# Kernel tuning notes

Measured on AMD Instinct MI355X. Metric: run time of the kernel, lower is better.

Reference implementation:

```python
import jax, jax.numpy as jnp
import numpy as np

NUM_HEADS = 16
KERNEL_SIZE = 13


def setup_inputs() -> dict:
    key = jax.random.key(0)
    ks = jax.random.split(key, 6)
    B, L, C = 4, 4096, 512
    H, K = NUM_HEADS, KERNEL_SIZE
    x = jax.random.normal(ks[0], (B, L, C), dtype=jnp.float32)
    qkv_w = jax.random.normal(ks[1], (C, 3 * C), dtype=jnp.float32) * 0.02
    qkv_b = jnp.zeros((3 * C,), dtype=jnp.float32)
    rpb = jax.random.normal(ks[2], (H, 2 * K - 1), dtype=jnp.float32) * 0.02
    proj_w = jax.random.normal(ks[3], (C, C), dtype=jnp.float32) * 0.02
    proj_b = jnp.zeros((C,), dtype=jnp.float32)
    return {"x": x, "qkv_w": qkv_w, "qkv_b": qkv_b, "rpb": rpb,
            "proj_w": proj_w, "proj_b": proj_b}


def reference(x, qkv_w, qkv_b, rpb, proj_w, proj_b):
    B, L, C = x.shape
    H, K = NUM_HEADS, KERNEL_SIZE
    hd = C // H
    scale = hd ** -0.5
    kh = K // 2

    # qkv projection -> q,k,v each [B,H,L,hd]
    qkv = (x @ qkv_w + qkv_b).reshape(B, L, 3, H, hd).transpose(2, 0, 3, 1, 4)
    q, k, v = qkv[0] * scale, qkv[1], qkv[2]

    # NATTEN window: start index clamped so window stays in-bounds
    pos = jnp.arange(L)
    ni = jnp.clip(pos - kh, 0, L - K)              # [L] window start per query
    idx = ni[:, None] + jnp.arange(K)[None, :]     # [L,K] key positions
    # rpb index: (key_pos - query_pos) + (K-1)
    rpb_idx = (ni - pos + (K - 1))[:, None] + jnp.arange(K)[None, :]  # [L,K]

    k_win = k[:, :, idx, :]                        # [B,H,L,K,hd]
    v_win = v[:, :, idx, :]                        # [B,H,L,K,hd]

    attn = jnp.einsum('bhld,bhlkd->bhlk', q, k_win) + rpb[:, rpb_idx][None]
    attn = jax.nn.softmax(attn, axis=-1)

    out = jnp.einsum('bhlk,bhlkd->bhld', attn, v_win)  # [B,H,L,hd]
    out = out.transpose(0, 2, 1, 3).reshape(B, L, C)
    return out @ proj_w + proj_b
```

## Files before the change

kernel.cpp:

```cpp
#include <hip/hip_runtime.h>
#include <hip/hip_bf16.h>
#include <stdint.h>


typedef __attribute__((ext_vector_type(8))) short short8;
typedef __attribute__((ext_vector_type(4))) float f32x4;
typedef __attribute__((ext_vector_type(8))) unsigned short u16x8;
typedef __attribute__((ext_vector_type(4))) float float4v;

#define NB 4
#define NL 4096
#define NC 512
#define NH 16
#define HD 32
#define KW 13
#define KHALF 6
#define NM (NB*NL)

__device__ __forceinline__ float b2f(unsigned short u) {
  union { unsigned int i; float f; } x; x.i = ((unsigned int)u) << 16; return x.f;
}
__device__ __forceinline__ unsigned short f2b(float f) {
  __hip_bfloat16 h = __float2bfloat16(f);
  return __builtin_bit_cast(unsigned short, h);
}
__device__ __forceinline__ void gll16(const unsigned short* g, unsigned short* l) {
  __builtin_amdgcn_global_load_lds(
      (const __attribute__((address_space(1))) void*)g,
      (__attribute__((address_space(3))) void*)l, 16, 0, 0);
}

__global__ __launch_bounds__(256) void cvt_f32_bf16(const float* __restrict__ in,
                                                    unsigned short* __restrict__ out) {
  long i = (long)blockIdx.x * 256 + threadIdx.x;
  const float4v* in4 = (const float4v*)in;
  float4v a = in4[i * 2];
  float4v b = in4[i * 2 + 1];
  u16x8 u;
  u[0] = f2b(a.x); u[1] = f2b(a.y); u[2] = f2b(a.z); u[3] = f2b(a.w);
  u[4] = f2b(b.x); u[5] = f2b(b.y); u[6] = f2b(b.z); u[7] = f2b(b.w);
  ((u16x8*)out)[i] = u;
}

__global__ __launch_bounds__(256) void transpose_bf16(const float* __restrict__ in,
                                                      unsigned short* __restrict__ out,
                                                      int R, int C) {
  __shared__ float t[32][33];
  int c0 = blockIdx.x * 32;
  int r0 = blockIdx.y * 32;
  int tx = threadIdx.x;
  int ty = threadIdx.y;
  #pragma unroll
  for (int i = ty; i < 32; i += 8)
    t[i][tx] = in[(long)(r0 + i) * C + c0 + tx];
  __syncthreads();
  #pragma unroll
  for (int i = ty; i < 32; i += 8)
    out[(long)(c0 + i) * R + r0 + tx] = f2b(t[tx][i]);
}


__device__ __forceinline__ void stage_half(const unsigned short* __restrict__ G,
                                           long rowBase, int K, int kt,
                                           unsigned short* ldsDst, int tid) {
  int r  = tid >> 3;
  int ch = (tid & 7) ^ (r & 7);
  const unsigned short* s0 = G + (rowBase + r) * (long)K + kt * 64 + ch * 8;
  gll16(s0, ldsDst + tid * 8);
  gll16(s0 + 64 * (long)K, ldsDst + 4096 + tid * 8);
}

#define BAR() __builtin_amdgcn_s_barrier()
#define LGK0() asm volatile("s_waitcnt lgkmcnt(0)" ::: "memory")
#define VM(N) asm volatile("s_waitcnt vmcnt(" #N ")" ::: "memory")

#define DS_A(ABASE, QM) do { \
  const char* _ba = (const char*)(ABASE); \
  _Pragma("unroll") for (int ii = 0; ii < 2; ++ii) { \
    int _row = wm*64 + ((QM)*2+ii)*16 + lr; \
    _Pragma("unroll") for (int kb = 0; kb < 2; ++kb) \
      af[ii][kb] = *(const short8*)(_ba + _row*128 + (((kb*4+lk) ^ lr7) * 16)); \
  } \
} while (0)

#define DS_B(BBASE, QN, BF) do { \
  const char* _bb = (const char*)(BBASE); \
  _Pragma("unroll") for (int jj = 0; jj < 2; ++jj) { \
    int _row = wn*64 + ((QN)*2+jj)*16 + lr; \
    _Pragma("unroll") for (int kb = 0; kb < 2; ++kb) \
      BF[jj][kb] = *(const short8*)(_bb + _row*128 + (((kb*4+lk) ^ lr7) * 16)); \
  } \
} while (0)

#define MMA(QM, QN, BF) do { \
  __builtin_amdgcn_s_setprio(1); \
  _Pragma("unroll") for (int ii = 0; ii < 2; ++ii) \
    _Pragma("unroll") for (int jj = 0; jj < 2; ++jj) \
      _Pragma("unroll") for (int kb = 0; kb < 2; ++kb) \
        acc[(QM)*2+ii][(QN)*2+jj] = __builtin_amdgcn_mfma_f32_16x16x32_bf16( \
            af[ii][kb], BF[jj][kb], acc[(QM)*2+ii][(QN)*2+jj], 0, 0, 0); \
  __builtin_amdgcn_s_setprio(0); \
} while (0)

template<int OUT_BF16>
__global__ __launch_bounds__(512, 2)
void gemm256(const unsigned short* __restrict__ A,
             const unsigned short* __restrict__ BT,
             const float* __restrict__ bias,
             void* __restrict__ Cout,
             int M, int N, int K, int tilesN) {
  __shared__ __align__(16) unsigned short lds[73728];

  int tid = threadIdx.x;
  int nwg = gridDim.x;
  int cpx = nwg >> 3;
  int wg  = ((int)blockIdx.x & 7) * cpx + ((int)blockIdx.x >> 3);
  int tm = wg / tilesN, tn = wg % tilesN;
  long mBase = (long)tm * 256;
  long nBase = (long)tn * 128;

  int lane = tid & 63, wave = tid >> 6;
  int wm = wave >> 1;
  int wn = wave & 1;
  int lr = lane & 15, lk = lane >> 4, lr7 = lr & 7;

  f32x4 acc[4][4];
  #pragma unroll
  for (int i = 0; i < 4; ++i)
    #pragma unroll
    for (int j = 0; j < 4; ++j) acc[i][j] = (f32x4){0.f, 0.f, 0.f, 0.f};

  short8 af[2][2], bf0[2][2], bf1[2][2];

  {
    unsigned short* A0 = lds;
    unsigned short* B0 = lds + 49152;
    unsigned short* A1 = lds + 16384;
    unsigned short* B1 = lds + 49152 + 8192;
    stage_half(A,  mBase,       K, 0, A0,        tid);
    stage_half(A,  mBase + 128, K, 0, A0 + 8192, tid);
    stage_half(BT, nBase,       K, 0, B0,        tid);
    stage_half(A,  mBase,       K, 1, A1,        tid);
    stage_half(A,  mBase + 128, K, 1, A1 + 8192, tid);
    stage_half(BT, nBase,       K, 1, B1,        tid);
  }
  VM(6);
  BAR();

  int bc = 0;
  #pragma unroll 1
  for (int kt = 0; kt < 8; ++kt) {
    int bs = bc == 0 ? 2 : bc - 1;
    unsigned short* A_cur = lds + bc * 16384;
    unsigned short* B_cur = lds + 49152 + bc * 8192;
    unsigned short* A_stg = lds + bs * 16384;
    unsigned short* B_stg = lds + 49152 + bs * 8192;
    bool st = (kt + 2) < 8;

    DS_A(A_cur, 0);
    DS_B(B_cur, 0, bf0);
    DS_B(B_cur, 1, bf1);
    if (st) {
      stage_half(A, mBase,       K, kt + 2, A_stg,        tid);
      stage_half(A, mBase + 128, K, kt + 2, A_stg + 8192, tid);
    }
    BAR(); LGK0();
    MMA(0, 0, bf0);
    MMA(0, 1, bf1);
    BAR();
    DS_A(A_cur, 1);
    if (st) stage_half(BT, nBase, K, kt + 2, B_stg, tid);
    BAR(); LGK0();
    MMA(1, 1, bf1);
    MMA(1, 0, bf0);
    if (st)              VM(6);
    else if (kt + 1 < 8) VM(0);
    BAR();
    bc = bc == 2 ? 0 : bc + 1;
  }

  long rowb = mBase + wm * 64 + (lane >> 4) * 4;
  int  colb = (int)nBase + wn * 64 + lr;
  if (OUT_BF16) {
    unsigned short* C = (unsigned short*)Cout;
    #pragma unroll
    for (int mi = 0; mi < 4; ++mi)
      #pragma unroll
      for (int nj = 0; nj < 4; ++nj) {
        int col = colb + nj * 16;
        float bv = bias[col];
        #pragma unroll
        for (int r = 0; r < 4; ++r)
          C[(rowb + mi * 16 + r) * (long)N + col] = f2b(acc[mi][nj][r] + bv);
      }
  } else {
    float* C = (float*)Cout;
    #pragma unroll
    for (int mi = 0; mi < 4; ++mi)
      #pragma unroll
      for (int nj = 0; nj < 4; ++nj) {
        int col = colb + nj * 16;
        float bv = bias[col];
        #pragma unroll
        for (int r = 0; r < 4; ++r)
          C[(rowb + mi * 16 + r) * (long)N + col] = acc[mi][nj][r] + bv;
      }
  }
}

__global__ __launch_bounds__(256)
void natt(const unsigned short* __restrict__ qkv, const float* __restrict__ rpb,
          unsigned short* __restrict__ out) {
  int tid = blockIdx.x * 256 + threadIdx.x;
  int h = tid & 15;
  int l = (tid >> 4) & (NL - 1);
  int b = tid >> 16;
  const float scale = 0.17677669529663687f;

  long qb = ((long)(b * NL + l) * 3) * NC + h * HD;
  float q[HD];
  {
    const u16x8* q8 = (const u16x8*)(qkv + qb);
    #pragma unroll
    for (int w = 0; w < 4; ++w) {
      u16x8 u = q8[w];
      #pragma unroll
      for (int e = 0; e < 8; ++e) q[w * 8 + e] = b2f(u[e]) * scale;
    }
  }

  int ni = l - KHALF;
  if (ni < 0) ni = 0;
  if (ni > NL - KW) ni = NL - KW;
  const float* rb = rpb + h * (2 * KW - 1) + (ni - l + KW - 1);

  float p[KW];
  float mx = -1e30f;
  #pragma unroll
  for (int j = 0; j < KW; ++j) {
    long kb = ((long)(b * NL + ni + j) * 3 + 1) * NC + h * HD;
    const u16x8* k8 = (const u16x8*)(qkv + kb);
    float s = 0.f;
    #pragma unroll
    for (int w = 0; w < 4; ++w) {
      u16x8 u = k8[w];
      #pragma unroll
      for (int e = 0; e < 8; ++e) s += q[w * 8 + e] * b2f(u[e]);
    }
    s += rb[j];
    p[j] = s;
    mx = fmaxf(mx, s);
  }

  float sum = 0.f;
  #pragma unroll
  for (int j = 0; j < KW; ++j) { p[j] = __expf(p[j] - mx); sum += p[j]; }
  float inv = 1.0f / sum;

  float o[HD];
  #pragma unroll
  for (int d = 0; d < HD; ++d) o[d] = 0.f;
  #pragma unroll
  for (int j = 0; j < KW; ++j) {
    long vb = ((long)(b * NL + ni + j) * 3 + 2) * NC + h * HD;
    const u16x8* v8 = (const u16x8*)(qkv + vb);
    float wj = p[j] * inv;
    #pragma unroll
    for (int w = 0; w < 4; ++w) {
      u16x8 u = v8[w];
      #pragma unroll
      for (int e = 0; e < 8; ++e) o[w * 8 + e] += wj * b2f(u[e]);
    }
  }

  unsigned short* op = out + (long)(b * NL + l) * NC + h * HD;
  #pragma unroll
  for (int w = 0; w < 4; ++w) {
    u16x8 u;
    #pragma unroll
    for (int e = 0; e < 8; ++e) u[e] = f2b(o[w * 8 + e]);
    *((u16x8*)(op + w * 8)) = u;
  }
}

extern "C" void kernel_launch(void* const* d_in, const int* in_sizes, int n_in,
                              void* d_out, int out_size, void* d_ws, size_t ws_size,
                              hipStream_t stream) {
  const float* x      = (const float*)d_in[0];
  const float* qkv_w  = (const float*)d_in[1];
  const float* qkv_b  = (const float*)d_in[2];
  const float* rpb    = (const float*)d_in[3];
  const float* proj_w = (const float*)d_in[4];
  const float* proj_b = (const float*)d_in[5];
  float* out = (float*)d_out;

  char* ws = (char*)d_ws;
  unsigned short* xb     = (unsigned short*)(ws);
  unsigned short* qkvwT  = (unsigned short*)(ws + 16777216);
  unsigned short* projwT = (unsigned short*)(ws + 18350080);
  unsigned short* qkvo   = (unsigned short*)(ws + 18874368);
  unsigned short* attno  = (unsigned short*)(ws + 69206016);

  cvt_f32_bf16<<<dim3(4096), dim3(256), 0, stream>>>(x, xb);
  transpose_bf16<<<dim3(48, 16), dim3(32, 8), 0, stream>>>(qkv_w, qkvwT, 512, 1536);
  transpose_bf16<<<dim3(16, 16), dim3(32, 8), 0, stream>>>(proj_w, projwT, 512, 512);
  gemm256<1><<<dim3(768), dim3(512), 0, stream>>>(xb, qkvwT, qkv_b, qkvo,
                                                  NM, 1536, 512, 12);
  natt<<<dim3(1024), dim3(256), 0, stream>>>(qkvo, rpb, attno);
  gemm256<0><<<dim3(256), dim3(512), 0, stream>>>(attno, projwT, proj_b, out,
                                                  NM, 512, 512, 4);
}
```

Measured before the change: 106.9 us.

## Replace 256x128 GEMM with 128x128 double-buffered tile and simpler k-loop

```diff
diff --git a/kernel.cpp b/kernel.cpp
--- a/kernel.cpp
+++ b/kernel.cpp
@@ -60,63 +60,78 @@
 }
 
 
-__device__ __forceinline__ void stage_half(const unsigned short* __restrict__ G,
+__device__ __forceinline__ void stage_tile(const unsigned short* __restrict__ G,
                                            long rowBase, int K, int kt,
                                            unsigned short* ldsDst, int tid) {
   int r  = tid >> 3;
   int ch = (tid & 7) ^ (r & 7);
   const unsigned short* s0 = G + (rowBase + r) * (long)K + kt * 64 + ch * 8;
-  gll16(s0, ldsDst + tid * 8);
-  gll16(s0 + 64 * (long)K, ldsDst + 4096 + tid * 8);
+  unsigned short* d0 = ldsDst + tid * 8;
+  #pragma unroll
+  for (int q = 0; q < 4; ++q)
+    gll16(s0 + (long)32 * q * K, d0 + 2048 * q);
 }
 
 #define BAR() __builtin_amdgcn_s_barrier()
-#define LGK0() asm volatile("s_waitcnt lgkmcnt(0)" ::: "memory")
+#define LGK0() do { asm volatile("s_waitcnt lgkmcnt(0)" ::: "memory"); \
+                    __builtin_amdgcn_sched_barrier(0); } while (0)
 #define VM(N) asm volatile("s_waitcnt vmcnt(" #N ")" ::: "memory")
 
-#define DS_A(ABASE, QM) do { \
+#define LDA(ABASE) do { \
   const char* _ba = (const char*)(ABASE); \
-  _Pragma("unroll") for (int ii = 0; ii < 2; ++ii) { \
-    int _row = wm*64 + ((QM)*2+ii)*16 + lr; \
+  _Pragma("unroll") for (int ii = 0; ii < 4; ++ii) { \
+    int _row = wm*64 + ii*16 + lr; \
     _Pragma("unroll") for (int kb = 0; kb < 2; ++kb) \
       af[ii][kb] = *(const short8*)(_ba + _row*128 + (((kb*4+lk) ^ lr7) * 16)); \
   } \
 } while (0)
 
-#define DS_B(BBASE, QN, BF) do { \
+#define LDB(BBASE) do { \
   const char* _bb = (const char*)(BBASE); \
-  _Pragma("unroll") for (int jj = 0; jj < 2; ++jj) { \
-    int _row = wn*64 + ((QN)*2+jj)*16 + lr; \
+  _Pragma("unroll") for (int jj = 0; jj < 4; ++jj) { \
+    int _row = wn*64 + jj*16 + lr; \
     _Pragma("unroll") for (int kb = 0; kb < 2; ++kb) \
-      BF[jj][kb] = *(const short8*)(_bb + _row*128 + (((kb*4+lk) ^ lr7) * 16)); \
+      bf[jj][kb] = *(const short8*)(_bb + _row*128 + (((kb*4+lk) ^ lr7) * 16)); \
   } \
 } while (0)
 
-#define MMA(QM, QN, BF) do { \
+#define MMA_ALL() do { \
   __builtin_amdgcn_s_setprio(1); \
-  _Pragma("unroll") for (int ii = 0; ii < 2; ++ii) \
-    _Pragma("unroll") for (int jj = 0; jj < 2; ++jj) \
+  _Pragma("unroll") for (int ii = 0; ii < 4; ++ii) \
+    _Pragma("unroll") for (int jj = 0; jj < 4; ++jj) \
       _Pragma("unroll") for (int kb = 0; kb < 2; ++kb) \
-        acc[(QM)*2+ii][(QN)*2+jj] = __builtin_amdgcn_mfma_f32_16x16x32_bf16( \
-            af[ii][kb], BF[jj][kb], acc[(QM)*2+ii][(QN)*2+jj], 0, 0, 0); \
+        acc[ii][jj] = __builtin_amdgcn_mfma_f32_16x16x32_bf16( \
+            af[ii][kb], bf[jj][kb], acc[ii][jj], 0, 0, 0); \
   __builtin_amdgcn_s_setprio(0); \
 } while (0)
 
+#define KTILE(AB, BB, KT, STG, VMARG) do { \
+  LDA(AB); LDB(BB); LGK0(); \
+  BAR(); \
+  if (STG) { \
+    stage_tile(Ag, mBase, K, (KT) + 2, AB, tid); \
+    stage_tile(Bg, nBase, K, (KT) + 2, BB, tid); \
+  } \
+  MMA_ALL(); \
+  VMARG; \
+  BAR(); \
+} while (0)
+
 template<int OUT_BF16>
-__global__ __launch_bounds__(512, 2)
-void gemm256(const unsigned short* __restrict__ A,
-             const unsigned short* __restrict__ BT,
+__global__ __launch_bounds__(256, 2)
+void gemm128(const unsigned short* __restrict__ Ag,
+             const unsigned short* __restrict__ Bg,
              const float* __restrict__ bias,
              void* __restrict__ Cout,
              int M, int N, int K, int tilesN) {
-  __shared__ __align__(16) unsigned short lds[73728];
+  __shared__ __align__(16) unsigned short lds[32768];
 
   int tid = threadIdx.x;
   int nwg = gridDim.x;
   int cpx = nwg >> 3;
   int wg  = ((int)blockIdx.x & 7) * cpx + ((int)blockIdx.x >> 3);
   int tm = wg / tilesN, tn = wg % tilesN;
-  long mBase = (long)tm * 256;
+  long mBase = (long)tm * 128;
   long nBase = (long)tn * 128;
 
   int lane = tid & 63, wave = tid >> 6;
@@ -124,59 +139,36 @@
   int wn = wave & 1;
   int lr = lane & 15, lk = lane >> 4, lr7 = lr & 7;
 
+  unsigned short* A0 = lds;
+  unsigned short* A1 = lds + 8192;
+  unsigned short* B0 = lds + 16384;
+  unsigned short* B1 = lds + 24576;
+
   f32x4 acc[4][4];
   #pragma unroll
   for (int i = 0; i < 4; ++i)
     #pragma unroll
     for (int j = 0; j < 4; ++j) acc[i][j] = (f32x4){0.f, 0.f, 0.f, 0.f};
 
-  short8 af[2][2], bf0[2][2], bf1[2][2];
-
-  {
-    unsigned short* A0 = lds;
-    unsigned short* B0 = lds + 49152;
-    unsigned short* A1 = lds + 16384;
-    unsigned short* B1 = lds + 49152 + 8192;
-    stage_half(A,  mBase,       K, 0, A0,        tid);
-    stage_half(A,  mBase + 128, K, 0, A0 + 8192, tid);
-    stage_half(BT, nBase,       K, 0, B0,        tid);
-    stage_half(A,  mBase,       K, 1, A1,        tid);
-    stage_half(A,  mBase + 128, K, 1, A1 + 8192, tid);
-    stage_half(BT, nBase,       K, 1, B1,        tid);
-  }
-  VM(6);
+  short8 af[4][2], bf[4][2];
+
+  stage_tile(Ag, mBase, K, 0, A0, tid);
+  stage_tile(Bg, nBase, K, 0, B0, tid);
+  stage_tile(Ag, mBase, K, 1, A1, tid);
+  stage_tile(Bg, nBase, K, 1, B1, tid);
+  VM(8);
   BAR();
 
-  int bc = 0;
   #pragma unroll 1
-  for (int kt = 0; kt < 8; ++kt) {
-    int bs = bc == 0 ? 2 : bc - 1;
-    unsigned short* A_cur = lds + bc * 16384;
-    unsigned short* B_cur = lds + 49152 + bc * 8192;
-    unsigned short* A_stg = lds + bs * 16384;
-    unsigned short* B_stg = lds + 49152 + bs * 8192;
-    bool st = (kt + 2) < 8;
-
-    DS_A(A_cur, 0);
-    DS_B(B_cur, 0, bf0);
-    DS_B(B_cur, 1, bf1);
-    if (st) {
-      stage_half(A, mBase,       K, kt + 2, A_stg,        tid);
-      stage_half(A, mBase + 128, K, kt + 2, A_stg + 8192, tid);
+  for (int i = 0; i < 4; ++i) {
+    int kt = 2 * i;
+    if (i < 3) {
+      KTILE(A0, B0, kt,     true,  VM(8));
+      KTILE(A1, B1, kt + 1, true,  VM(8));
+    } else {
+      KTILE(A0, B0, kt,     false, VM(0));
+      KTILE(A1, B1, kt + 1, false, (void)0);
     }
-    BAR(); LGK0();
-    MMA(0, 0, bf0);
-    MMA(0, 1, bf1);
-    BAR();
-    DS_A(A_cur, 1);
-    if (st) stage_half(BT, nBase, K, kt + 2, B_stg, tid);
-    BAR(); LGK0();
-    MMA(1, 1, bf1);
-    MMA(1, 0, bf0);
-    if (st)              VM(6);
-    else if (kt + 1 < 8) VM(0);
-    BAR();
-    bc = bc == 2 ? 0 : bc + 1;
   }
 
   long rowb = mBase + wm * 64 + (lane >> 4) * 4;
@@ -304,9 +296,9 @@
   cvt_f32_bf16<<<dim3(4096), dim3(256), 0, stream>>>(x, xb);
   transpose_bf16<<<dim3(48, 16), dim3(32, 8), 0, stream>>>(qkv_w, qkvwT, 512, 1536);
   transpose_bf16<<<dim3(16, 16), dim3(32, 8), 0, stream>>>(proj_w, projwT, 512, 512);
-  gemm256<1><<<dim3(768), dim3(512), 0, stream>>>(xb, qkvwT, qkv_b, qkvo,
-                                                  NM, 1536, 512, 12);
+  gemm128<1><<<dim3(1536), dim3(256), 0, stream>>>(xb, qkvwT, qkv_b, qkvo,
+                                                   NM, 1536, 512, 12);
   natt<<<dim3(1024), dim3(256), 0, stream>>>(qkvo, rpb, attno);
-  gemm256<0><<<dim3(256), dim3(512), 0, stream>>>(attno, projwT, proj_b, out,
+  gemm128<0><<<dim3(512), dim3(256), 0, stream>>>(attno, projwT, proj_b, out,
                                                   NM, 512, 512, 4);
 }
```

Result: faster. 101.6 us (-4.9%).
